# Performance work log

Hardware: AMD Instinct MI355X
Metric: run time of the kernel (lower is better)

The kernel has to match this reference:

```python
import jax, jax.numpy as jnp
import numpy as np

M = 16384          # test points
N = 16384          # train points
D = 2              # (kx, ky)
CHUNK = 8192       # rows of K_star per chunk (matches torch default)


def setup_inputs() -> dict:
    key = jax.random.key(0)
    k1, k2, k3 = jax.random.split(key, 3)
    X_test = jax.random.normal(k1, (M, D), dtype=jnp.float32)
    X_train = jax.random.normal(k2, (N, D), dtype=jnp.float32)
    alpha = jax.random.normal(k3, (N, 2), dtype=jnp.float32)  # dual vars [Re, Im]
    log_lengthscale = jnp.asarray(np.log(0.1), dtype=jnp.float32)
    log_outputscale = jnp.asarray(np.log(1.0), dtype=jnp.float32)
    return {
        "X_test": X_test,
        "X_train": X_train,
        "alpha": alpha,
        "log_lengthscale": log_lengthscale,
        "log_outputscale": log_outputscale,
    }


def reference(X_test, X_train, alpha, log_lengthscale, log_outputscale):
    """Posterior mean mu* = K_rbf(X_test, X_train) @ alpha, chunked over test rows."""
    ell2 = jnp.exp(log_lengthscale) ** 2
    sf2 = jnp.exp(log_outputscale) ** 2
    xt_sq = jnp.sum(X_train * X_train, axis=1)  # (N,)

    def chunk_fn(xc):  # xc: (CHUNK, D)
        # squared euclidean distances (clamped at 0 for numerical safety)
        sq = (jnp.sum(xc * xc, axis=1)[:, None]
              + xt_sq[None, :]
              - 2.0 * (xc @ X_train.T))          # (CHUNK, N)
        sq = jnp.maximum(sq, 0.0)
        K = sf2 * jnp.exp(-0.5 * sq / ell2)      # RBF kernel values
        return K @ alpha                          # (CHUNK, 2)

    m = X_test.shape[0]
    chunks = X_test.reshape(m // CHUNK, CHUNK, D)
    out = jax.lax.map(chunk_fn, chunks)           # (m//CHUNK, CHUNK, 2)
    return out.reshape(m, 2)
```

## Files before the change

kernel.cpp:

```cpp
#include <hip/hip_runtime.h>
#include <math.h>

#define M_PTS 16384
#define N_PTS 16384

#define NC 42
#define NCELLS (NC * NC)
#define NPAIR (NCELLS / 2)
#define H 0.25f
#define INV_H 4.0f
#define ORIG (-5.25f)
#define TCUT 20.0f
#define KCAP 31

#define OFF_HTR 0
#define OFF_TRS (OFF_HTR + NCELLS * 4)
#define OFF_TRCUR (OFF_TRS + (NCELLS + 1) * 4 + 60)
#define OFF_TRA ((OFF_TRCUR + NCELLS * 4 + 255) & ~255)
#define OFF_TRW1 (OFF_TRA + N_PTS * 16)
#define WS_NEED (OFF_TRW1 + (size_t)N_PTS * 4)

__device__ __forceinline__ float fexp2(float x) {
#if __has_builtin(__builtin_amdgcn_exp2f)
    return __builtin_amdgcn_exp2f(x);
#else
    return exp2f(x);
#endif
}

__device__ __forceinline__ void gatomic_fadd(float* p, float v) {
    asm volatile("global_atomic_add_f32 %0, %1, off" :: "v"(p), "v"(v) : "memory");
}

__device__ __forceinline__ int cellco(float v) {
    int c = (int)floorf((v - ORIG) * INV_H);
    return min(NC - 1, max(0, c));
}

__global__ __launch_bounds__(256) void hist_kernel(
        const float2* __restrict__ Xtr, int* __restrict__ hTr) {
    int i = blockIdx.x * 256 + threadIdx.x;
    float2 t = Xtr[i];
    atomicAdd(&hTr[cellco(t.y) * NC + cellco(t.x)], 1);
}

__global__ __launch_bounds__(1024) void scan_kernel(
        const int* __restrict__ hTr, int* __restrict__ trs,
        int* __restrict__ trcur) {
    __shared__ int sc[1024];
    const int tid = threadIdx.x;
    int hv0 = (tid < NPAIR) ? hTr[2 * tid] : 0;
    int hv1 = (tid < NPAIR) ? hTr[2 * tid + 1] : 0;
    int v = hv0 + hv1;
    sc[tid] = v; __syncthreads();
    for (int o = 1; o < 1024; o <<= 1) {
        int u = (tid >= o) ? sc[tid - o] : 0;
        __syncthreads(); sc[tid] += u; __syncthreads();
    }
    if (tid < NPAIR) {
        int e = sc[tid] - v;
        trs[2 * tid] = e;      trcur[2 * tid] = e;
        trs[2 * tid + 1] = e + hv0;  trcur[2 * tid + 1] = e + hv0;
    }
    if (tid == NPAIR - 1) trs[NCELLS] = sc[tid];
}

__global__ __launch_bounds__(256) void scatter_kernel(
        const float2* __restrict__ Xtr, const float2* __restrict__ alpha,
        const float* __restrict__ log_ell, const float* __restrict__ log_sf,
        int* __restrict__ trcur, float4* __restrict__ trA,
        float* __restrict__ trW1) {
    int i = blockIdx.x * 256 + threadIdx.x;
    float ell = expf(log_ell[0]);
    float sf2 = expf(2.0f * log_sf[0]);
    float c = -0.5f / (ell * ell) * 1.4426950408889634f;

    float2 t = Xtr[i];
    float2 a = alpha[i];
    int ct = cellco(t.y) * NC + cellco(t.x);
    int pt = atomicAdd(&trcur[ct], 1);
    trA[pt] = make_float4(-2.f * c * t.x, -2.f * c * t.y,
                          c * (t.x * t.x + t.y * t.y), sf2 * a.x);
    trW1[pt] = sf2 * a.y;
}

__global__ __launch_bounds__(256) void gp_point(
        const float2* __restrict__ Xte, const float4* __restrict__ trA,
        const float* __restrict__ trW1, const int* __restrict__ trs,
        const float* __restrict__ log_ell, float2* __restrict__ out2) {
    const int wid = (blockIdx.x << 2) + (threadIdx.x >> 6);
    const int lane = threadIdx.x & 63;

    const float ell = expf(log_ell[0]);
    const float cmag = 0.5f / (ell * ell) * 1.4426950408889634f;
    const float r2 = TCUT / cmag;

    const float2 xt = Xte[wid];
    const float b = -cmag * (xt.x * xt.x + xt.y * xt.y);

    int K = (int)floorf(sqrtf(r2) * INV_H) + 1;
    int js_l = 0, je_l = 0;
    int nrows;
    if (K > KCAP) {
        nrows = 1;
        if (lane == 0) { js_l = 0; je_l = N_PTS; }
    } else {
        nrows = 2 * K + 1;
        const int cx = cellco(xt.x), cy = cellco(xt.y);
        if (lane < nrows) {
            int ry = cy - K + lane;
            if (ry >= 0 && ry < NC) {
                int dy = (lane < K) ? (K - lane) : (lane - K);
                int kx;
                if (dy <= 1) kx = K;
                else {
                    float d = (float)(dy - 1) * H;
                    kx = (int)floorf(sqrtf(fmaxf(r2 - d * d, 0.f)) * INV_H) + 1;
                }
                int c0 = max(0, cx - kx);
                int c1 = min(NC - 1, cx + kx);
                js_l = trs[ry * NC + c0];
                je_l = trs[ry * NC + c1 + 1];
            }
        }
    }

    float a0 = 0.f, a1 = 0.f;
    for (int rr = 0; rr < nrows; ++rr) {
        const int js = __shfl(js_l, rr);
        const int je = __shfl(je_l, rr);
        for (int j0 = js; j0 < je; j0 += 64) {
            int j = j0 + lane;
            int jc = min(j, je - 1);
            float4 tv = trA[jc];
            float w1 = trW1[jc];
            float arg = fmaf(tv.x, xt.x, fmaf(tv.y, xt.y, b + tv.z));
            arg = (j < je) ? arg : -1.0e30f;
            float e = fexp2(arg);
            a0 = fmaf(e, tv.w, a0);
            a1 = fmaf(e, w1, a1);
        }
    }

    for (int o = 32; o > 0; o >>= 1) {
        a0 += __shfl_xor(a0, o);
        a1 += __shfl_xor(a1, o);
    }
    if (lane == 0) out2[wid] = make_float2(a0, a1);
}

__global__ __launch_bounds__(256, 8) void gp_dense(
        const float2* __restrict__ Xte, const float2* __restrict__ Xtr,
        const float2* __restrict__ alpha, const float* __restrict__ log_ell,
        const float* __restrict__ log_sf, float* __restrict__ out) {
    __shared__ float4 sSt[128];
    __shared__ float sA1[128];
    const int tid = threadIdx.x;
    const float ell = expf(log_ell[0]);
    const float c = -0.5f / (ell * ell) * 1.4426950408889634f;
    const int j0 = blockIdx.y * 128;
    if (tid < 128) {
        const float sf2 = expf(2.0f * log_sf[0]);
        float2 t = Xtr[j0 + tid];
        float2 a = alpha[j0 + tid];
        sSt[tid] = make_float4(-2.f * c * t.x, -2.f * c * t.y,
                               c * (t.x * t.x + t.y * t.y), sf2 * a.x);
        sA1[tid] = sf2 * a.y;
    }
    const int base = blockIdx.x * 1024 + tid;
    float2 x0 = Xte[base], x1 = Xte[base + 256];
    float2 x2 = Xte[base + 512], x3 = Xte[base + 768];
    const float b0 = c * (x0.x * x0.x + x0.y * x0.y);
    const float b1 = c * (x1.x * x1.x + x1.y * x1.y);
    const float b2 = c * (x2.x * x2.x + x2.y * x2.y);
    const float b3 = c * (x3.x * x3.x + x3.y * x3.y);
    __syncthreads();
    float a00 = 0.f, a01 = 0.f, a10 = 0.f, a11 = 0.f;
    float a20 = 0.f, a21 = 0.f, a30 = 0.f, a31 = 0.f;
#pragma unroll 2
    for (int j = 0; j < 128; ++j) {
        float4 s = sSt[j];
        float w1 = sA1[j];
        float e0 = fexp2(fminf(fmaf(s.x, x0.x, fmaf(s.y, x0.y, b0 + s.z)), 0.f));
        float e1 = fexp2(fminf(fmaf(s.x, x1.x, fmaf(s.y, x1.y, b1 + s.z)), 0.f));
        float e2 = fexp2(fminf(fmaf(s.x, x2.x, fmaf(s.y, x2.y, b2 + s.z)), 0.f));
        float e3 = fexp2(fminf(fmaf(s.x, x3.x, fmaf(s.y, x3.y, b3 + s.z)), 0.f));
        a00 = fmaf(e0, s.w, a00); a01 = fmaf(e0, w1, a01);
        a10 = fmaf(e1, s.w, a10); a11 = fmaf(e1, w1, a11);
        a20 = fmaf(e2, s.w, a20); a21 = fmaf(e2, w1, a21);
        a30 = fmaf(e3, s.w, a30); a31 = fmaf(e3, w1, a31);
    }
    gatomic_fadd(&out[2 * base], a00);            gatomic_fadd(&out[2 * base + 1], a01);
    gatomic_fadd(&out[2 * (base + 256)], a10);    gatomic_fadd(&out[2 * (base + 256) + 1], a11);
    gatomic_fadd(&out[2 * (base + 512)], a20);    gatomic_fadd(&out[2 * (base + 512) + 1], a21);
    gatomic_fadd(&out[2 * (base + 768)], a30);    gatomic_fadd(&out[2 * (base + 768) + 1], a31);
}

extern "C" void kernel_launch(void* const* d_in, const int* in_sizes, int n_in,
                              void* d_out, int out_size, void* d_ws, size_t ws_size,
                              hipStream_t stream) {
    const float2* Xte = (const float2*)d_in[0];
    const float2* Xtr = (const float2*)d_in[1];
    const float2* alpha = (const float2*)d_in[2];
    const float* log_ell = (const float*)d_in[3];
    const float* log_sf = (const float*)d_in[4];
    float* out = (float*)d_out;

    if (ws_size >= WS_NEED) {
        char* ws = (char*)d_ws;
        int* hTr = (int*)(ws + OFF_HTR);
        int* trs = (int*)(ws + OFF_TRS);
        int* trcur = (int*)(ws + OFF_TRCUR);
        float4* trA = (float4*)(ws + OFF_TRA);
        float* trW1 = (float*)(ws + OFF_TRW1);

        hipMemsetAsync(hTr, 0, NCELLS * sizeof(int), stream);
        hist_kernel<<<N_PTS / 256, 256, 0, stream>>>(Xtr, hTr);
        scan_kernel<<<1, 1024, 0, stream>>>(hTr, trs, trcur);
        scatter_kernel<<<N_PTS / 256, 256, 0, stream>>>(Xtr, alpha, log_ell,
                                                        log_sf, trcur, trA, trW1);
        gp_point<<<M_PTS / 4, 256, 0, stream>>>(Xte, trA, trW1, trs, log_ell,
                                                (float2*)out);
    } else {
        hipMemsetAsync(out, 0, (size_t)out_size * sizeof(float), stream);
        dim3 grid(M_PTS / 1024, N_PTS / 128);
        gp_dense<<<grid, 256, 0, stream>>>(Xte, Xtr, alpha, log_ell, log_sf, out);
    }
}
```

Measured before the change: 118.8 us.

## Bin test points into spatial tiles and process tile-chunk work items

Test points are now also sorted into cells with a blocked key, so each 64-point group is spatially compact. The plan kernel computes one shared neighbour-cell window per group and splits the training candidates into 64-wide work items. A wave loads each candidate chunk once into LDS and evaluates it against all 64 test points, with partial sums combined by atomics. This replaces per-test-point cell walks and their divergent, redundant global loads. The shared window is wider than each point's own window, so more exp evaluations run, and per-item atomics are added. Histogramming is moved to per-block shared memory.

```diff
diff --git a/kernel.cpp b/kernel.cpp
--- a/kernel.cpp
+++ b/kernel.cpp
@@ -11,14 +11,25 @@
 #define INV_H 4.0f
 #define ORIG (-5.25f)
 #define TCUT 20.0f
-#define KCAP 31
-
-#define OFF_HTR 0
-#define OFF_TRS (OFF_HTR + NCELLS * 4)
-#define OFF_TRCUR (OFF_TRS + (NCELLS + 1) * 4 + 60)
-#define OFF_TRA ((OFF_TRCUR + NCELLS * 4 + 255) & ~255)
+
+#define NTG 256
+#define GROWS 42
+#define NPART 16
+#define MAXITEMS 65536
+#define MAIN_BLOCKS 4096
+
+#define OFF_PTR 0
+#define OFF_PTE (OFF_PTR + NPART * NCELLS * 4)
+#define OFF_TRCUR (OFF_PTE + NPART * NCELLS * 4)
+#define OFF_TECUR (OFF_TRCUR + NCELLS * 4)
+#define OFF_NIT ((OFF_TECUR + NCELLS * 4 + 255) & ~255)
+#define OFF_GOFF (OFF_NIT + 256)
+#define OFF_GPRE (OFF_GOFF + NTG * GROWS * 4)
+#define OFF_ITEMS (OFF_GPRE + NTG * (GROWS + 1) * 4)
+#define OFF_TRA ((OFF_ITEMS + MAXITEMS * 4 + 255) & ~255)
 #define OFF_TRW1 (OFF_TRA + N_PTS * 16)
-#define WS_NEED (OFF_TRW1 + (size_t)N_PTS * 4)
+#define OFF_T4 ((OFF_TRW1 + N_PTS * 4 + 255) & ~255)
+#define WS_NEED (OFF_T4 + (size_t)M_PTS * 16)
 
 __device__ __forceinline__ float fexp2(float x) {
 #if __has_builtin(__builtin_amdgcn_exp2f)
@@ -37,21 +48,59 @@
     return min(NC - 1, max(0, c));
 }
 
-__global__ __launch_bounds__(256) void hist_kernel(
-        const float2* __restrict__ Xtr, int* __restrict__ hTr) {
-    int i = blockIdx.x * 256 + threadIdx.x;
+__device__ __forceinline__ int bkey(int cx, int cy) {
+    int t = cy >> 2;
+    int ht = (t == 10) ? 2 : 4;
+    return t * 168 + cx * ht + (cy & 3);
+}
+
+__global__ __launch_bounds__(1024) void histpart_kernel(
+        const float2* __restrict__ Xtr, const float2* __restrict__ Xte,
+        int* __restrict__ pTr, int* __restrict__ pTe,
+        float2* __restrict__ out2) {
+    __shared__ int hT[NCELLS], hE[NCELLS];
+    const int tid = threadIdx.x, blk = blockIdx.x;
+    for (int i = tid; i < NCELLS; i += 1024) { hT[i] = 0; hE[i] = 0; }
+    __syncthreads();
+    int i = blk * 1024 + tid;
     float2 t = Xtr[i];
-    atomicAdd(&hTr[cellco(t.y) * NC + cellco(t.x)], 1);
-}
-
-__global__ __launch_bounds__(1024) void scan_kernel(
-        const int* __restrict__ hTr, int* __restrict__ trs,
-        int* __restrict__ trcur) {
+    atomicAdd(&hT[cellco(t.y) * NC + cellco(t.x)], 1);
+    float2 x = Xte[i];
+    atomicAdd(&hE[bkey(cellco(x.x), cellco(x.y))], 1);
+    out2[i] = make_float2(0.f, 0.f);
+    __syncthreads();
+    for (int c = tid; c < NCELLS; c += 1024) {
+        pTr[blk * NCELLS + c] = hT[c];
+        pTe[blk * NCELLS + c] = hE[c];
+    }
+}
+
+__global__ __launch_bounds__(1024) void scanplan_kernel(
+        const int* __restrict__ pTr, const int* __restrict__ pTe,
+        const float* __restrict__ log_ell,
+        int* __restrict__ trcur, int* __restrict__ tecur,
+        int* __restrict__ gOff, int* __restrict__ gPre,
+        int* __restrict__ items, int* __restrict__ nitG) {
     __shared__ int sc[1024];
+    __shared__ int trsL[NCELLS + 1];
+    __shared__ int tesL[NCELLS + 1];
     const int tid = threadIdx.x;
-    int hv0 = (tid < NPAIR) ? hTr[2 * tid] : 0;
-    int hv1 = (tid < NPAIR) ? hTr[2 * tid + 1] : 0;
-    int v = hv0 + hv1;
+    if (tid == 0) nitG[0] = 0;
+
+    __shared__ int hT[NCELLS], hE[NCELLS];
+    for (int c = tid; c < NCELLS; c += 1024) {
+        int sT = 0, sE = 0;
+        for (int p = 0; p < NPART; ++p) {
+            sT += pTr[p * NCELLS + c];
+            sE += pTe[p * NCELLS + c];
+        }
+        hT[c] = sT; hE[c] = sE;
+    }
+    __syncthreads();
+
+    int v0 = (tid < NPAIR) ? hT[2 * tid] : 0;
+    int v1 = (tid < NPAIR) ? hT[2 * tid + 1] : 0;
+    int v = v0 + v1;
     sc[tid] = v; __syncthreads();
     for (int o = 1; o < 1024; o <<= 1) {
         int u = (tid >= o) ? sc[tid - o] : 0;
@@ -59,94 +108,204 @@
     }
     if (tid < NPAIR) {
         int e = sc[tid] - v;
-        trs[2 * tid] = e;      trcur[2 * tid] = e;
-        trs[2 * tid + 1] = e + hv0;  trcur[2 * tid + 1] = e + hv0;
-    }
-    if (tid == NPAIR - 1) trs[NCELLS] = sc[tid];
+        trsL[2 * tid] = e;
+        trsL[2 * tid + 1] = e + v0;
+    }
+    if (tid == NPAIR - 1) trsL[NCELLS] = sc[tid];
+    __syncthreads();
+    v0 = (tid < NPAIR) ? hE[2 * tid] : 0;
+    v1 = (tid < NPAIR) ? hE[2 * tid + 1] : 0;
+    v = v0 + v1;
+    sc[tid] = v; __syncthreads();
+    for (int o = 1; o < 1024; o <<= 1) {
+        int u = (tid >= o) ? sc[tid - o] : 0;
+        __syncthreads(); sc[tid] += u; __syncthreads();
+    }
+    if (tid < NPAIR) {
+        int e = sc[tid] - v;
+        tesL[2 * tid] = e;
+        tesL[2 * tid + 1] = e + v0;
+    }
+    if (tid == NPAIR - 1) tesL[NCELLS] = sc[tid];
+    __syncthreads();
+
+    for (int c = tid; c < NCELLS; c += 1024) {
+        trcur[c] = trsL[c];
+        tecur[c] = tesL[c];
+    }
+    __syncthreads();
+
+    if (tid < NTG) {
+        const int g = tid;
+        const float ell = expf(log_ell[0]);
+        const float cmag = 0.5f / (ell * ell) * 1.4426950408889634f;
+        const float r2 = TCUT / cmag;
+        const int K = (int)floorf(sqrtf(r2) * INV_H) + 1;
+
+        int ka, kb;
+        {
+            int s = g * 64, lo = 0, hi = NCELLS;
+            while (lo + 1 < hi) { int m = (lo + hi) >> 1; if (tesL[m] <= s) lo = m; else hi = m; }
+            ka = lo;
+            s = g * 64 + 63; lo = 0; hi = NCELLS;
+            while (lo + 1 < hi) { int m = (lo + hi) >> 1; if (tesL[m] <= s) lo = m; else hi = m; }
+            kb = lo;
+        }
+        int bx0, bx1, by0, by1;
+        {
+            int ta = ka / 168, tb = kb / 168;
+            int hta = (ta == 10) ? 2 : 4;
+            int ra = ka - ta * 168, rb = kb - tb * 168;
+            int cxa = ra / hta;
+            if (ta == tb) {
+                int cxb = rb / hta;
+                bx0 = cxa; bx1 = cxb;
+                if (cxa == cxb) {
+                    by0 = 4 * ta + (ra - cxa * hta);
+                    by1 = 4 * ta + (rb - cxb * hta);
+                } else {
+                    by0 = 4 * ta;
+                    by1 = min(NC - 1, 4 * ta + hta - 1);
+                }
+            } else {
+                bx0 = 0; bx1 = NC - 1;
+                int htb = (tb == 10) ? 2 : 4;
+                by0 = 4 * ta;
+                by1 = min(NC - 1, 4 * tb + htb - 1);
+            }
+        }
+
+        const int ry0 = max(0, by0 - K), ry1 = min(NC - 1, by1 + K);
+        int W = 0, idx = 0;
+        gPre[g * (GROWS + 1)] = 0;
+        for (int ry = ry0; ry <= ry1; ++ry, ++idx) {
+            int dy = max(max(by0 - ry, ry - by1), 0);
+            int kx;
+            if (dy <= 1) kx = K;
+            else {
+                float d = (float)(dy - 1) * H;
+                kx = (int)floorf(sqrtf(fmaxf(r2 - d * d, 0.f)) * INV_H) + 1;
+            }
+            int c0 = max(0, bx0 - kx);
+            int c1 = min(NC - 1, bx1 + kx);
+            int js = trsL[ry * NC + c0];
+            int je = trsL[ry * NC + c1 + 1];
+            gOff[g * GROWS + idx] = js - W;
+            W += je - js;
+            gPre[g * (GROWS + 1) + idx + 1] = W;
+        }
+        for (int i2 = idx; i2 < GROWS; ++i2)
+            gPre[g * (GROWS + 1) + i2 + 1] = W;
+
+        const int nch = (W + 63) >> 6;
+        int base = atomicAdd(nitG, nch);
+        int r = 0;
+        for (int k = 0; k < nch; ++k) {
+            int start = k << 6;
+            while (r < GROWS - 1 && start >= gPre[g * (GROWS + 1) + r + 1]) ++r;
+            items[base + k] = g | (k << 8) | (r << 16);
+        }
+    }
 }
 
 __global__ __launch_bounds__(256) void scatter_kernel(
-        const float2* __restrict__ Xtr, const float2* __restrict__ alpha,
-        const float* __restrict__ log_ell, const float* __restrict__ log_sf,
-        int* __restrict__ trcur, float4* __restrict__ trA,
-        float* __restrict__ trW1) {
-    int i = blockIdx.x * 256 + threadIdx.x;
-    float ell = expf(log_ell[0]);
-    float sf2 = expf(2.0f * log_sf[0]);
-    float c = -0.5f / (ell * ell) * 1.4426950408889634f;
-
-    float2 t = Xtr[i];
-    float2 a = alpha[i];
-    int ct = cellco(t.y) * NC + cellco(t.x);
-    int pt = atomicAdd(&trcur[ct], 1);
-    trA[pt] = make_float4(-2.f * c * t.x, -2.f * c * t.y,
-                          c * (t.x * t.x + t.y * t.y), sf2 * a.x);
-    trW1[pt] = sf2 * a.y;
-}
-
-__global__ __launch_bounds__(256) void gp_point(
-        const float2* __restrict__ Xte, const float4* __restrict__ trA,
-        const float* __restrict__ trW1, const int* __restrict__ trs,
-        const float* __restrict__ log_ell, float2* __restrict__ out2) {
-    const int wid = (blockIdx.x << 2) + (threadIdx.x >> 6);
+        const float2* __restrict__ Xtr, const float2* __restrict__ Xte,
+        const float2* __restrict__ alpha, const float* __restrict__ log_ell,
+        const float* __restrict__ log_sf,
+        int* __restrict__ trcur, int* __restrict__ tecur,
+        float4* __restrict__ trA, float* __restrict__ trW1,
+        float4* __restrict__ T4) {
+    const int bid = blockIdx.x;
+    const float ell = expf(log_ell[0]);
+    const float c = -0.5f / (ell * ell) * 1.4426950408889634f;
+    if (bid < 64) {
+        int i = bid * 256 + threadIdx.x;
+        const float sf2 = expf(2.0f * log_sf[0]);
+        float2 t = Xtr[i];
+        float2 a = alpha[i];
+        int ct = cellco(t.y) * NC + cellco(t.x);
+        int pt = atomicAdd(&trcur[ct], 1);
+        trA[pt] = make_float4(-2.f * c * t.x, -2.f * c * t.y,
+                              c * (t.x * t.x + t.y * t.y), sf2 * a.x);
+        trW1[pt] = sf2 * a.y;
+    } else {
+        int i = (bid - 64) * 256 + threadIdx.x;
+        float2 x = Xte[i];
+        int key = bkey(cellco(x.x), cellco(x.y));
+        int px = atomicAdd(&tecur[key], 1);
+        T4[px] = make_float4(x.x, x.y, c * (x.x * x.x + x.y * x.y),
+                             __int_as_float(i));
+    }
+}
+
+__global__ __launch_bounds__(256, 8) void gp_item(
+        const float4* __restrict__ T4, const float4* __restrict__ trA,
+        const float* __restrict__ trW1, const int* __restrict__ gOff,
+        const int* __restrict__ gPre, const int* __restrict__ items,
+        const int* __restrict__ nitG, float* __restrict__ out) {
+    __shared__ float4 sA[4][64];
+    __shared__ __align__(16) float sW[4][64];
+    __shared__ int sPre[4][GROWS + 2];
+    __shared__ int sOff[4][GROWS];
+
+    const int wv = threadIdx.x >> 6;
     const int lane = threadIdx.x & 63;
-
-    const float ell = expf(log_ell[0]);
-    const float cmag = 0.5f / (ell * ell) * 1.4426950408889634f;
-    const float r2 = TCUT / cmag;
-
-    const float2 xt = Xte[wid];
-    const float b = -cmag * (xt.x * xt.x + xt.y * xt.y);
-
-    int K = (int)floorf(sqrtf(r2) * INV_H) + 1;
-    int js_l = 0, je_l = 0;
-    int nrows;
-    if (K > KCAP) {
-        nrows = 1;
-        if (lane == 0) { js_l = 0; je_l = N_PTS; }
-    } else {
-        nrows = 2 * K + 1;
-        const int cx = cellco(xt.x), cy = cellco(xt.y);
-        if (lane < nrows) {
-            int ry = cy - K + lane;
-            if (ry >= 0 && ry < NC) {
-                int dy = (lane < K) ? (K - lane) : (lane - K);
-                int kx;
-                if (dy <= 1) kx = K;
-                else {
-                    float d = (float)(dy - 1) * H;
-                    kx = (int)floorf(sqrtf(fmaxf(r2 - d * d, 0.f)) * INV_H) + 1;
-                }
-                int c0 = max(0, cx - kx);
-                int c1 = min(NC - 1, cx + kx);
-                js_l = trs[ry * NC + c0];
-                je_l = trs[ry * NC + c1 + 1];
-            }
-        }
-    }
-
-    float a0 = 0.f, a1 = 0.f;
-    for (int rr = 0; rr < nrows; ++rr) {
-        const int js = __shfl(js_l, rr);
-        const int je = __shfl(je_l, rr);
-        for (int j0 = js; j0 < je; j0 += 64) {
-            int j = j0 + lane;
-            int jc = min(j, je - 1);
-            float4 tv = trA[jc];
-            float w1 = trW1[jc];
-            float arg = fmaf(tv.x, xt.x, fmaf(tv.y, xt.y, b + tv.z));
-            arg = (j < je) ? arg : -1.0e30f;
-            float e = fexp2(arg);
-            a0 = fmaf(e, tv.w, a0);
-            a1 = fmaf(e, w1, a1);
-        }
-    }
-
-    for (int o = 32; o > 0; o >>= 1) {
-        a0 += __shfl_xor(a0, o);
-        a1 += __shfl_xor(a1, o);
-    }
-    if (lane == 0) out2[wid] = make_float2(a0, a1);
+    const int nit = nitG[0];
+
+    for (int it = (blockIdx.x << 2) + wv; it < nit; it += MAIN_BLOCKS * 4) {
+        const int item = items[it];
+        const int g = item & 0xFF;
+        const int k = (item >> 8) & 0xFF;
+        const int r0 = (item >> 16) & 0x3F;
+
+        if (lane < GROWS) sOff[wv][lane] = gOff[g * GROWS + lane];
+        if (lane < GROWS + 1) sPre[wv][lane] = gPre[g * (GROWS + 1) + lane];
+        float4 tp = T4[(g << 6) + lane];
+        __builtin_amdgcn_wave_barrier();
+        asm volatile("" ::: "memory");
+
+        const int W = sPre[wv][GROWS];
+        const int gg = (k << 6) + lane;
+        float4 tv; float wvv;
+        if (gg < W) {
+            int r = r0;
+            while (r < GROWS - 1 && gg >= sPre[wv][r + 1]) ++r;
+            int j = gg + sOff[wv][r];
+            tv = trA[j];
+            wvv = trW1[j];
+        } else {
+            tv = make_float4(0.f, 0.f, -1.0e30f, 0.f);
+            wvv = 0.f;
+        }
+        sA[wv][lane] = tv;
+        sW[wv][lane] = wvv;
+        __builtin_amdgcn_wave_barrier();
+        asm volatile("" ::: "memory");
+
+        const float x = tp.x, y = tp.y, b = tp.z;
+        const int oi = __float_as_int(tp.w);
+        float a0 = 0.f, a1 = 0.f;
+#pragma unroll 4
+        for (int q = 0; q < 16; ++q) {
+            float4 t0 = sA[wv][4 * q];
+            float4 t1 = sA[wv][4 * q + 1];
+            float4 t2 = sA[wv][4 * q + 2];
+            float4 t3 = sA[wv][4 * q + 3];
+            float4 w4 = *(const float4*)&sW[wv][4 * q];
+            float e0 = fexp2(fmaf(t0.x, x, fmaf(t0.y, y, b + t0.z)));
+            float e1 = fexp2(fmaf(t1.x, x, fmaf(t1.y, y, b + t1.z)));
+            float e2 = fexp2(fmaf(t2.x, x, fmaf(t2.y, y, b + t2.z)));
+            float e3 = fexp2(fmaf(t3.x, x, fmaf(t3.y, y, b + t3.z)));
+            a0 = fmaf(e0, t0.w, a0); a1 = fmaf(e0, w4.x, a1);
+            a0 = fmaf(e1, t1.w, a0); a1 = fmaf(e1, w4.y, a1);
+            a0 = fmaf(e2, t2.w, a0); a1 = fmaf(e2, w4.z, a1);
+            a0 = fmaf(e3, t3.w, a0); a1 = fmaf(e3, w4.w, a1);
+        }
+        gatomic_fadd(&out[2 * oi], a0);
+        gatomic_fadd(&out[2 * oi + 1], a1);
+        __builtin_amdgcn_wave_barrier();
+        asm volatile("" ::: "memory");
+    }
 }
 
 __global__ __launch_bounds__(256, 8) void gp_dense(
@@ -208,19 +367,26 @@
 
     if (ws_size >= WS_NEED) {
         char* ws = (char*)d_ws;
-        int* hTr = (int*)(ws + OFF_HTR);
-        int* trs = (int*)(ws + OFF_TRS);
+        int* pTr = (int*)(ws + OFF_PTR);
+        int* pTe = (int*)(ws + OFF_PTE);
         int* trcur = (int*)(ws + OFF_TRCUR);
+        int* tecur = (int*)(ws + OFF_TECUR);
+        int* nitG = (int*)(ws + OFF_NIT);
+        int* gOff = (int*)(ws + OFF_GOFF);
+        int* gPre = (int*)(ws + OFF_GPRE);
+        int* items = (int*)(ws + OFF_ITEMS);
         float4* trA = (float4*)(ws + OFF_TRA);
         float* trW1 = (float*)(ws + OFF_TRW1);
-
-        hipMemsetAsync(hTr, 0, NCELLS * sizeof(int), stream);
-        hist_kernel<<<N_PTS / 256, 256, 0, stream>>>(Xtr, hTr);
-        scan_kernel<<<1, 1024, 0, stream>>>(hTr, trs, trcur);
-        scatter_kernel<<<N_PTS / 256, 256, 0, stream>>>(Xtr, alpha, log_ell,
-                                                        log_sf, trcur, trA, trW1);
-        gp_point<<<M_PTS / 4, 256, 0, stream>>>(Xte, trA, trW1, trs, log_ell,
-                                                (float2*)out);
+        float4* T4 = (float4*)(ws + OFF_T4);
+
+        histpart_kernel<<<NPART, 1024, 0, stream>>>(Xtr, Xte, pTr, pTe,
+                                                    (float2*)out);
+        scanplan_kernel<<<1, 1024, 0, stream>>>(pTr, pTe, log_ell, trcur, tecur,
+                                                gOff, gPre, items, nitG);
+        scatter_kernel<<<128, 256, 0, stream>>>(Xtr, Xte, alpha, log_ell, log_sf,
+                                                trcur, tecur, trA, trW1, T4);
+        gp_item<<<MAIN_BLOCKS, 256, 0, stream>>>(T4, trA, trW1, gOff, gPre,
+                                                 items, nitG, out);
     } else {
         hipMemsetAsync(out, 0, (size_t)out_size * sizeof(float), stream);
         dim3 grid(M_PTS / 1024, N_PTS / 128);
```

Result: slower. 271.7 us (+128.6%).
